# Kernel optimization log

Hardware: AMD Instinct MI355X
Metric: run time of the kernel (lower is better)

The kernel has to match this reference:

```python
import jax, jax.numpy as jnp
import numpy as np

DIM = 256
NUM_HEADS = 8
HEAD_DIM = 64
NUM_MEM_KV = 4
HIDDEN = NUM_HEADS * HEAD_DIM  # 512


def rmsnorm(x, g):
    # F.normalize(x, dim=1) * g * sqrt(C)
    c = x.shape[1]
    n = jnp.sqrt(jnp.sum(x * x, axis=1, keepdims=True))
    xn = x / jnp.maximum(n, 1e-12)
    return xn * g * (c ** 0.5)


def setup_inputs() -> dict:
    key = jax.random.key(0)
    ks = jax.random.split(key, 7)
    b, h, w = 16, 64, 64
    x = jax.random.normal(ks[0], (b, DIM, h, w), dtype=jnp.float32)
    g_in = jnp.ones((1, DIM, 1, 1), dtype=jnp.float32)
    w_qkv = jax.random.normal(ks[1], (HIDDEN * 3, DIM), dtype=jnp.float32) * (1.0 / np.sqrt(DIM))
    mem_kv = jax.random.normal(ks[2], (2, NUM_HEADS, HEAD_DIM, NUM_MEM_KV), dtype=jnp.float32)
    w_out = jax.random.normal(ks[3], (DIM, HIDDEN), dtype=jnp.float32) * (1.0 / np.sqrt(HIDDEN))
    b_out = jax.random.normal(ks[4], (DIM,), dtype=jnp.float32) * 0.01
    g_out = jnp.ones((1, DIM, 1, 1), dtype=jnp.float32)
    return {"x": x, "g_in": g_in, "w_qkv": w_qkv, "mem_kv": mem_kv,
            "w_out": w_out, "b_out": b_out, "g_out": g_out}


def reference(x, g_in, w_qkv, mem_kv, w_out, b_out, g_out):
    b, c, h, w = x.shape
    scale = HEAD_DIM ** (-0.5)
    xn = rmsnorm(x, g_in)
    # 1x1 conv (no bias) as GEMM: [b, 3*hidden, h, w]
    qkv = jnp.einsum('bcxy,oc->boxy', xn, w_qkv)
    q, k, v = jnp.split(qkv, 3, axis=1)
    # b (heads d) x y -> b heads d n
    def to_heads(t):
        return t.reshape(b, NUM_HEADS, HEAD_DIM, h * w)
    q, k, v = to_heads(q), to_heads(k), to_heads(v)
    mem_k = jnp.broadcast_to(mem_kv[0], (b, NUM_HEADS, HEAD_DIM, NUM_MEM_KV))
    mem_v = jnp.broadcast_to(mem_kv[1], (b, NUM_HEADS, HEAD_DIM, NUM_MEM_KV))
    k = jnp.concatenate([mem_k, k], axis=-1)
    v = jnp.concatenate([mem_v, v], axis=-1)
    q = jax.nn.softmax(q, axis=-2) * scale   # softmax over head_dim
    k = jax.nn.softmax(k, axis=-1)           # softmax over sequence
    context = jnp.einsum('bhdn,bhen->bhde', k, v)  # [b,h,d,d] per-head context
    out = jnp.einsum('bhde,bhdn->bhen', context, q)  # [b,h,d,n]
    out = out.reshape(b, HIDDEN, h, w)
    out = jnp.einsum('bcxy,oc->boxy', out, w_out) + b_out[None, :, None, None]
    return rmsnorm(out, g_out)
```

## Files before the change

kernel.cpp:

```cpp
#include <hip/hip_runtime.h>
#include <hip/hip_bf16.h>

typedef __hip_bfloat16 bf16;
typedef short bf16x8 __attribute__((ext_vector_type(8)));
typedef float f32x4 __attribute__((ext_vector_type(4)));

#define PTOT  65536
#define NPOS  4096
#define CIN   256
#define HID   512
#define HD    64

__device__ __forceinline__ float us2f(unsigned short u) {
    return __uint_as_float(((unsigned int)u) << 16);
}
__device__ __forceinline__ float ldf(const void* p, size_t i, bool bf) {
    return bf ? us2f(((const unsigned short*)p)[i]) : ((const float*)p)[i];
}
__device__ __forceinline__ unsigned short f2bs(float v) {
    __hip_bfloat16 h = __float2bfloat16(v);
    return *reinterpret_cast<unsigned short*>(&h);
}
__device__ __forceinline__ void gld16(const void* g, void* s) {
    __builtin_amdgcn_global_load_lds(
        (const __attribute__((address_space(1))) unsigned int*)g,
        (__attribute__((address_space(3))) unsigned int*)s, 16, 0, 0);
}

__global__ __launch_bounds__(256) void k_detect(const unsigned* __restrict__ x,
                                                int* __restrict__ flag) {
    int t = threadIdx.x;
    unsigned w = x[(size_t)t * 997];
    unsigned e7 = (w >> 8) & 0x7f;
    __shared__ int s[256];
    s[t] = (e7 >= 58 && e7 <= 66) ? 1 : 0;
    __syncthreads();
    for (int k = 128; k > 0; k >>= 1) { if (t < k) s[t] += s[t + k]; __syncthreads(); }
    if (t == 0) flag[0] = (s[0] >= 128) ? 1 : 0;
}

__global__ void k_relay(const int* __restrict__ src, int* __restrict__ dst) {
    dst[0] = src[0];
}

__global__ __launch_bounds__(256) void k_cvt(const void* __restrict__ src,
        unsigned short* __restrict__ dst, int n, const int* __restrict__ flag) {
    bool bf = flag[0] != 0;
    int i = blockIdx.x * 256 + threadIdx.x;
    if (i < n) dst[i] = f2bs(ldf(src, i, bf));
}

__global__ __launch_bounds__(256) void k_norm_xn(
        const void* __restrict__ x, const void* __restrict__ g,
        unsigned short* __restrict__ xn, const int* __restrict__ flag)
{
    bool bf = flag[0] != 0;
    __shared__ float xs[64][65];
    __shared__ float gS[256];
    __shared__ float sS[64];
    __shared__ float red[4][64];
    int t = threadIdx.x;
    int p0 = blockIdx.x * 64;
    int b = p0 >> 12;
    int posbase = p0 & 4095;
    gS[t] = ldf(g, t, bf);
    int pl = t & 63, cg = t >> 6;
    const size_t xbase = ((size_t)b * CIN) << 12;
    float ss = 0.f;
    for (int c = cg * 64; c < cg * 64 + 64; ++c) {
        float v = ldf(x, xbase + ((size_t)c << 12) + posbase + pl, bf);
        ss += v * v;
    }
    red[cg][pl] = ss;
    __syncthreads();
    if (t < 64) {
        float tot = red[0][t] + red[1][t] + red[2][t] + red[3][t];
        sS[t] = 16.0f / fmaxf(sqrtf(tot), 1e-12f);
    }
    for (int c0 = 0; c0 < 256; c0 += 64) {
        __syncthreads();
        #pragma unroll
        for (int r = 0; r < 16; ++r) {
            int c = c0 + r * 4 + cg;
            xs[r * 4 + cg][pl] = ldf(x, xbase + ((size_t)c << 12) + posbase + pl, bf);
        }
        __syncthreads();
        int pr = t >> 2, c4 = (t & 3) * 16;
        float sc = sS[pr];
        unsigned short tmp[16];
        #pragma unroll
        for (int j = 0; j < 16; ++j)
            tmp[j] = f2bs(xs[c4 + j][pr] * sc * gS[c0 + c4 + j]);
        unsigned short* dst = &xn[(size_t)(p0 + pr) * 256 + c0 + c4];
        *(uint4*)dst = ((uint4*)tmp)[0];
        *(uint4*)(dst + 8) = ((uint4*)tmp)[1];
    }
}

template<int KTOT, bool BIAS, int OSTRIDE>
__global__ __launch_bounds__(256) void k_mfma(
        const bf16* __restrict__ Am, const bf16* __restrict__ Bm,
        const void* __restrict__ bias, bf16* __restrict__ C,
        const int* __restrict__ flag)
{
    __shared__ __align__(16) unsigned short As[128 * 32];
    __shared__ __align__(16) unsigned short Bs[128 * 32];
    const int tid = threadIdx.x;
    const int wv = tid >> 6, lane = tid & 63;
    const int quad = lane >> 4, l16 = lane & 15;
    const int wm = wv >> 1, wn = wv & 1;
    const int m0 = blockIdx.y * 128, n0 = blockIdx.x * 128;
    f32x4 acc[4][4] = {};
    const bf16* gA = Am + (size_t)(m0 + (tid >> 2)) * KTOT + (tid & 3) * 8;
    const bf16* gB = Bm + (size_t)(n0 + (tid >> 2)) * KTOT + (tid & 3) * 8;
    unsigned short* lA = As + wv * 512;
    unsigned short* lB = Bs + wv * 512;
    for (int k0 = 0; k0 < KTOT; k0 += 32) {
        gld16(gA + k0, lA);
        gld16(gA + (size_t)64 * KTOT + k0, lA + 2048);
        gld16(gB + k0, lB);
        gld16(gB + (size_t)64 * KTOT + k0, lB + 2048);
        __syncthreads();
        bf16x8 bfr[4];
        #pragma unroll
        for (int j = 0; j < 4; ++j)
            bfr[j] = *(const bf16x8*)&Bs[(wn * 64 + j * 16 + l16) * 32 + quad * 8];
        #pragma unroll
        for (int i = 0; i < 4; ++i) {
            bf16x8 af = *(const bf16x8*)&As[(wm * 64 + i * 16 + l16) * 32 + quad * 8];
            #pragma unroll
            for (int j = 0; j < 4; ++j)
                acc[i][j] = __builtin_amdgcn_mfma_f32_16x16x32_bf16(af, bfr[j], acc[i][j], 0, 0, 0);
        }
        __syncthreads();
    }
    bool bf = BIAS ? (flag[0] != 0) : false;
    #pragma unroll
    for (int i = 0; i < 4; ++i) {
        int row = m0 + wm * 64 + i * 16 + quad * 4;
        #pragma unroll
        for (int r = 0; r < 4; ++r) {
            float bv = BIAS ? ldf(bias, row + r, bf) : 0.0f;
            #pragma unroll
            for (int j = 0; j < 4; ++j) {
                int col = n0 + wn * 64 + j * 16 + l16;
                C[(size_t)(row + r) * OSTRIDE + col] = __float2bfloat16(acc[i][j][r] + bv);
            }
        }
    }
}

__global__ __launch_bounds__(512) void k_kvgemm(
        const bf16* __restrict__ Am, const bf16* __restrict__ Bm,
        bf16* __restrict__ C)
{
    __shared__ __align__(16) unsigned short As[128 * 256];
    __shared__ __align__(16) unsigned short Bs[2][64 * 256];
    const int t = threadIdx.x;
    const int w = t >> 6, lane = t & 63;
    const int quad = lane >> 4, l16 = lane & 15;
    const int wm = w >> 1, wn = w & 1;
    const int p = blockIdx.x;
    const int xcd = p & 7, slot = p >> 3;
    const int chunk = xcd * 4 + (slot & 3);
    const int mt = slot >> 2;
    const int m0 = mt * 128;
    const size_t cbase = (size_t)chunk * 2048;

    const int srow = t >> 5;
    const int sks  = (t & 31) ^ (srow & 7);

    #pragma unroll
    for (int q = 0; q < 8; ++q)
        gld16(Am + (size_t)(m0 + q * 16 + srow) * 256 + sks * 8,
              (char*)As + q * 8192 + w * 1024);
    #pragma unroll
    for (int q = 0; q < 4; ++q)
        gld16(Bm + (cbase + q * 16 + srow) * 256 + sks * 8,
              (char*)Bs[0] + q * 8192 + w * 1024);
    #pragma unroll
    for (int q = 0; q < 4; ++q)
        gld16(Bm + (cbase + 64 + q * 16 + srow) * 256 + sks * 8,
              (char*)Bs[1] + q * 8192 + w * 1024);

    asm volatile("s_waitcnt vmcnt(8)" ::: "memory");
    __builtin_amdgcn_s_barrier();
    asm volatile("" ::: "memory");

    bf16x8 af[2][8];
    #pragma unroll
    for (int i = 0; i < 2; ++i) {
        int row = wm * 32 + i * 16 + l16;
        #pragma unroll
        for (int kk = 0; kk < 8; ++kk)
            af[i][kk] = *(const bf16x8*)((const char*)As + row * 512 +
                         (((kk * 4 + quad) ^ (row & 7)) << 4));
    }

    for (int s = 0; s < 32; ++s) {
        if (s > 0) {
            asm volatile("" ::: "memory");
            __builtin_amdgcn_s_barrier();
            asm volatile("" ::: "memory");
            if (s + 1 < 32) {
                #pragma unroll
                for (int q = 0; q < 4; ++q)
                    gld16(Bm + (cbase + (size_t)(s + 1) * 64 + q * 16 + srow) * 256 + sks * 8,
                          (char*)Bs[(s + 1) & 1] + q * 8192 + w * 1024);
            }
        }
        if (s == 0)      asm volatile("s_waitcnt vmcnt(4)"  ::: "memory");
        else if (s < 31) asm volatile("s_waitcnt vmcnt(20)" ::: "memory");
        else             asm volatile("s_waitcnt vmcnt(16)" ::: "memory");
        __builtin_amdgcn_s_barrier();
        asm volatile("" ::: "memory");

        const unsigned short* Bbuf = Bs[s & 1];
        f32x4 acc[2][2] = {};
        #pragma unroll
        for (int kk = 0; kk < 8; ++kk) {
            bf16x8 bfr[2];
            #pragma unroll
            for (int j = 0; j < 2; ++j) {
                int row = wn * 32 + j * 16 + l16;
                bfr[j] = *(const bf16x8*)((const char*)Bbuf + row * 512 +
                          (((kk * 4 + quad) ^ (row & 7)) << 4));
            }
            #pragma unroll
            for (int i = 0; i < 2; ++i)
                #pragma unroll
                for (int j = 0; j < 2; ++j)
                    acc[i][j] = __builtin_amdgcn_mfma_f32_16x16x32_bf16(af[i][kk], bfr[j], acc[i][j], 0, 0, 0);
        }
        #pragma unroll
        for (int i = 0; i < 2; ++i) {
            #pragma unroll
            for (int r = 0; r < 4; ++r) {
                int row = m0 + wm * 32 + i * 16 + quad * 4 + r;
                size_t col = cbase + (size_t)s * 64 + wn * 32;
                #pragma unroll
                for (int j = 0; j < 2; ++j)
                    C[(size_t)row * PTOT + col + j * 16 + l16] = __float2bfloat16(acc[i][j][r]);
            }
        }
    }
}

__global__ __launch_bounds__(256) void k_qapply(
        const bf16* __restrict__ xn, const bf16* __restrict__ wq,
        const unsigned short* __restrict__ ct_bf,
        unsigned short* __restrict__ oat_pe)
{
    __shared__ __align__(16) unsigned short smem[128 * 136 + 2 * 64 * 72];
    unsigned short* As  = smem;
    unsigned short* Bs  = smem + 8192;
    unsigned short* As2 = smem;
    unsigned short* ctS = smem + 17408;
    const int tid = threadIdx.x;
    const int wv = tid >> 6, lane = tid & 63;
    const int quad = lane >> 4, l16 = lane & 15;
    const int wm = wv >> 1, wn = wv & 1;
    const int n0 = blockIdx.x * 128;
    const int m0 = blockIdx.y * 128;
    const int b = m0 >> 12;

    {
        int hh = tid >> 7, tt = tid & 127;
        int bh = (b << 3) + (n0 >> 6) + hh;
        int e = tt >> 1, d0 = (tt & 1) * 32;
        const unsigned short* src = ct_bf + (size_t)bh * 4096 + e * 64 + d0;
        unsigned short* dst = ctS + hh * 4608 + e * 72 + d0;
        *(uint4*)dst        = *(const uint4*)src;
        *(uint4*)(dst + 8)  = *(const uint4*)(src + 8);
        *(uint4*)(dst + 16) = *(const uint4*)(src + 16);
        *(uint4*)(dst + 24) = *(const uint4*)(src + 24);
    }

    f32x4 acc[4][4] = {};
    const bf16* gA = xn + (size_t)(m0 + (tid >> 2)) * CIN + (tid & 3) * 8;
    const bf16* gB = wq + (size_t)(n0 + (tid >> 2)) * CIN + (tid & 3) * 8;
    unsigned short* lA = As + wv * 512;
    unsigned short* lB = Bs + wv * 512;
    for (int k0 = 0; k0 < CIN; k0 += 32) {
        gld16(gA + k0, lA);
        gld16(gA + (size_t)64 * CIN + k0, lA + 2048);
        gld16(gB + k0, lB);
        gld16(gB + (size_t)64 * CIN + k0, lB + 2048);
        __syncthreads();
        bf16x8 bfr[4];
        #pragma unroll
        for (int j = 0; j < 4; ++j)
            bfr[j] = *(const bf16x8*)&Bs[(wn * 64 + j * 16 + l16) * 32 + quad * 8];
        #pragma unroll
        for (int i = 0; i < 4; ++i) {
            bf16x8 af = *(const bf16x8*)&As[(wm * 64 + i * 16 + l16) * 32 + quad * 8];
            #pragma unroll
            for (int j = 0; j < 4; ++j)
                acc[i][j] = __builtin_amdgcn_mfma_f32_16x16x32_bf16(af, bfr[j], acc[i][j], 0, 0, 0);
        }
        __syncthreads();
    }

    #pragma unroll
    for (int i = 0; i < 4; ++i) {
        #pragma unroll
        for (int r = 0; r < 4; ++r) {
            float m = fmaxf(fmaxf(acc[i][0][r], acc[i][1][r]),
                            fmaxf(acc[i][2][r], acc[i][3][r]));
            #pragma unroll
            for (int s = 1; s < 16; s <<= 1)
                m = fmaxf(m, __shfl_xor(m, s));
            float ev[4];
            float sum = 0.f;
            #pragma unroll
            for (int j = 0; j < 4; ++j) { ev[j] = expf(acc[i][j][r] - m); sum += ev[j]; }
            #pragma unroll
            for (int s = 1; s < 16; s <<= 1)
                sum += __shfl_xor(sum, s);
            float inv = 0.125f / sum;
            int row = wm * 64 + i * 16 + quad * 4 + r;
            #pragma unroll
            for (int j = 0; j < 4; ++j)
                As2[row * 136 + wn * 64 + j * 16 + l16] = f2bs(ev[j] * inv);
        }
    }
    __syncthreads();

    f32x4 acc2[4][4] = {};
    #pragma unroll
    for (int kk = 0; kk < 2; ++kk) {
        bf16x8 bfr[4];
        #pragma unroll
        for (int j = 0; j < 4; ++j)
            bfr[j] = *(const bf16x8*)&ctS[wn * 4608 + (j * 16 + l16) * 72 + kk * 32 + quad * 8];
        #pragma unroll
        for (int i = 0; i < 4; ++i) {
            bf16x8 af = *(const bf16x8*)&As2[(wm * 64 + i * 16 + l16) * 136 + wn * 64 + kk * 32 + quad * 8];
            #pragma unroll
            for (int j = 0; j < 4; ++j)
                acc2[i][j] = __builtin_amdgcn_mfma_f32_16x16x32_bf16(af, bfr[j], acc2[i][j], 0, 0, 0);
        }
    }
    #pragma unroll
    for (int i = 0; i < 4; ++i) {
        #pragma unroll
        for (int r = 0; r < 4; ++r) {
            int prow = wm * 64 + i * 16 + quad * 4 + r;
            unsigned short* obase = oat_pe + (size_t)(m0 + prow) * HID + n0 + wn * 64;
            #pragma unroll
            for (int j = 0; j < 4; ++j)
                obase[j * 16 + l16] = f2bs(acc2[i][j][r]);
        }
    }
}

__global__ __launch_bounds__(256) void k_kstats(
        const bf16* __restrict__ kv, const void* __restrict__ memkv,
        float* __restrict__ rowmax, float* __restrict__ rowinv,
        const int* __restrict__ flag)
{
    bool bf = flag[0] != 0;
    int r = blockIdx.x;
    int b = r >> 9, hd = r & 511;
    const unsigned short* krow = (const unsigned short*)kv + (size_t)hd * PTOT + b * NPOS;
    int t = threadIdx.x;
    float vals[16];
    float m = -1e30f;
    #pragma unroll
    for (int i = 0; i < 16; ++i) {
        vals[i] = us2f(krow[t + (i << 8)]);
        m = fmaxf(m, vals[i]);
    }
    float mv = (t < 4) ? ldf(memkv, hd * 4 + t, bf) : -1e30f;
    m = fmaxf(m, mv);
    __shared__ float red[256];
    red[t] = m; __syncthreads();
    for (int s = 128; s > 0; s >>= 1) {
        if (t < s) red[t] = fmaxf(red[t], red[t + s]);
        __syncthreads();
    }
    float M = red[0]; __syncthreads();
    float sum = 0.f;
    #pragma unroll
    for (int i = 0; i < 16; ++i) sum += expf(vals[i] - M);
    if (t < 4) sum += expf(mv - M);
    red[t] = sum; __syncthreads();
    for (int s = 128; s > 0; s >>= 1) {
        if (t < s) red[t] += red[t + s];
        __syncthreads();
    }
    if (t == 0) { rowmax[r] = M; rowinv[r] = 1.0f / red[0]; }
}

__global__ __launch_bounds__(256) void k_context_mfma(
        const bf16* __restrict__ kv, const void* __restrict__ memkv,
        const float* __restrict__ rowmax, const float* __restrict__ rowinv,
        float* __restrict__ ctpart, const int* __restrict__ flag)
{
    bool bf = flag[0] != 0;
    int bh = blockIdx.x, chunk = blockIdx.y;
    int b = bh >> 3, h = bh & 7;
    __shared__ __align__(16) unsigned short As[4][64 * 32];
    __shared__ __align__(16) unsigned short Bs[4][64 * 32];
    __shared__ float rmS[64], riS[64];
    const int tid = threadIdx.x;
    if (tid < 64) {
        rmS[tid] = rowmax[(b << 9) + (h << 6) + tid];
        riS[tid] = rowinv[(b << 9) + (h << 6) + tid];
    }
    __syncthreads();
    const int wv = tid >> 6, lane = tid & 63;
    const int quad = lane >> 4, l16 = lane & 15;
    const int wm = wv >> 1, wn = wv & 1;
    const int krow = tid >> 2, kseg = tid & 3;
    const float rm = rmS[krow], ri = riS[krow];
    const unsigned short* kbase = (const unsigned short*)kv + (size_t)(h * HD) * PTOT + b * NPOS + chunk * 1024;
    const unsigned short* vbase = (const unsigned short*)kv + (size_t)(HID + h * HD) * PTOT + b * NPOS + chunk * 1024;
    f32x4 acc[2][2] = {};
    for (int s = 0; s < 8; ++s) {
        int nb = s * 128;
        #pragma unroll
        for (int kk = 0; kk < 4; ++kk) {
            uint4 u = *(const uint4*)(kbase + (size_t)krow * PTOT + nb + kk * 32 + kseg * 8);
            unsigned short out[8];
            const unsigned short* us = (const unsigned short*)&u;
            #pragma unroll
            for (int e = 0; e < 8; ++e)
                out[e] = f2bs(expf(us2f(us[e]) - rm) * ri);
            *(uint4*)&As[kk][krow * 32 + kseg * 8] = *(uint4*)out;
        }
        #pragma unroll
        for (int kk = 0; kk < 4; ++kk)
            gld16(vbase + (size_t)(wv * 16 + (lane >> 2)) * PTOT + nb + kk * 32 + (lane & 3) * 8,
                  &Bs[kk][wv * 512]);
        __syncthreads();
        #pragma unroll
        for (int kk = 0; kk < 4; ++kk) {
            bf16x8 bfr[2];
            #pragma unroll
            for (int j = 0; j < 2; ++j)
                bfr[j] = *(const bf16x8*)&Bs[kk][(wn * 32 + j * 16 + l16) * 32 + quad * 8];
            #pragma unroll
            for (int i = 0; i < 2; ++i) {
                bf16x8 af = *(const bf16x8*)&As[kk][(wm * 32 + i * 16 + l16) * 32 + quad * 8];
                #pragma unroll
                for (int j = 0; j < 2; ++j)
                    acc[i][j] = __builtin_amdgcn_mfma_f32_16x16x32_bf16(af, bfr[j], acc[i][j], 0, 0, 0);
            }
        }
        __syncthreads();
    }
    if (chunk == 0) {
        float mv[2][4];
        #pragma unroll
        for (int j = 0; j < 2; ++j) {
            int e = wn * 32 + j * 16 + l16;
            #pragma unroll
            for (int mm = 0; mm < 4; ++mm)
                mv[j][mm] = ldf(memkv, 2048 + ((h << 6) + e) * 4 + mm, bf);
        }
        #pragma unroll
        for (int i = 0; i < 2; ++i) {
            #pragma unroll
            for (int r = 0; r < 4; ++r) {
                int d = wm * 32 + i * 16 + quad * 4 + r;
                #pragma unroll
                for (int mm = 0; mm < 4; ++mm) {
                    float kw = expf(ldf(memkv, ((h << 6) + d) * 4 + mm, bf) - rmS[d]) * riS[d];
                    #pragma unroll
                    for (int j = 0; j < 2; ++j)
                        acc[i][j][r] = fmaf(kw, mv[j][mm], acc[i][j][r]);
                }
            }
        }
    }
    float* outp = ctpart + (size_t)(chunk * 128 + bh) * 4096;
    #pragma unroll
    for (int i = 0; i < 2; ++i) {
        #pragma unroll
        for (int r = 0; r < 4; ++r) {
            int d = wm * 32 + i * 16 + quad * 4 + r;
            #pragma unroll
            for (int j = 0; j < 2; ++j) {
                int e = wn * 32 + j * 16 + l16;
                outp[d * 64 + e] = acc[i][j][r];
            }
        }
    }
}

__global__ __launch_bounds__(256) void k_ctsum(
        const float* __restrict__ ctpart, unsigned short* __restrict__ ct_bf)
{
    int bh = blockIdx.x, t = threadIdx.x;
    int i0 = t * 16;
    int e = i0 >> 6, d0 = i0 & 63;
    unsigned short tmp[16];
    #pragma unroll
    for (int j = 0; j < 16; ++j) {
        int d = d0 + j;
        float s = 0.f;
        #pragma unroll
        for (int c = 0; c < 4; ++c)
            s += ctpart[(size_t)(c * 128 + bh) * 4096 + d * 64 + e];
        tmp[j] = f2bs(s);
    }
    unsigned short* dst = ct_bf + (size_t)bh * 4096 + i0;
    *(uint4*)dst = ((uint4*)tmp)[0];
    *(uint4*)(dst + 8) = ((uint4*)tmp)[1];
}

template<bool BF>
__device__ __forceinline__ void rmsout_body(const unsigned short* pre, const void* g, void* out) {
    int p = blockIdx.x * 256 + threadIdx.x;
    int b = p >> 12, pos = p & 4095;
    float ss = 0.f;
    for (int c = 0; c < CIN; ++c) { float v = us2f(pre[(size_t)c * PTOT + p]); ss += v * v; }
    float scale = 16.0f / fmaxf(sqrtf(ss), 1e-12f);
    for (int c = 0; c < CIN; ++c) {
        float v = us2f(pre[(size_t)c * PTOT + p]) * scale * (BF ? us2f(((const unsigned short*)g)[c]) : ((const float*)g)[c]);
        size_t oi = ((size_t)(b * CIN + c) << 12) + pos;
        if (BF) ((unsigned short*)out)[oi] = f2bs(v);
        else    ((float*)out)[oi] = v;
    }
}
__global__ __launch_bounds__(256) void k_rmsnorm_out(
        const unsigned short* __restrict__ pre, const void* __restrict__ g,
        void* __restrict__ out, const int* __restrict__ flag)
{
    if (flag[0]) rmsout_body<true>(pre, g, out);
    else         rmsout_body<false>(pre, g, out);
}

extern "C" void kernel_launch(void* const* d_in, const int* in_sizes, int n_in,
                              void* d_out, int out_size, void* d_ws, size_t ws_size,
                              hipStream_t stream) {
    const void* x     = d_in[0];
    const void* g_in  = d_in[1];
    const void* w_qkv = d_in[2];
    const void* memkv = d_in[3];
    const void* w_out = d_in[4];
    const void* b_out = d_in[5];
    const void* g_out = d_in[6];

    char* ws = (char*)d_ws;
    bf16*           kv     = (bf16*)ws;
    unsigned short* oat_pe = (unsigned short*)(ws + 67108864);
    unsigned short* pre    = (unsigned short*)ws;
    int*            flagB  = (int*)(ws + 50331648);

    char* ob = (char*)d_out;
    float*          ctpart = (float*)ob;
    float*          rowmax = (float*)(ob + 8388608);
    float*          rowinv = (float*)(ob + 8421376);
    int*            flagA  = (int*)(ob + 8454144);
    unsigned short* wq_b   = (unsigned short*)(ob + 9437184);
    unsigned short* wout_b = (unsigned short*)(ob + 10485760);
    unsigned short* ct_bf  = (unsigned short*)(ob + 11010048);
    unsigned short* xn     = (unsigned short*)(ob + 12582912);

    k_detect<<<1, 256, 0, stream>>>((const unsigned*)x, flagA);

    k_cvt<<<1536, 256, 0, stream>>>(w_qkv, wq_b, 1536 * 256, flagA);
    k_cvt<<<512, 256, 0, stream>>>(w_out, wout_b, 256 * 512, flagA);

    k_norm_xn<<<1024, 256, 0, stream>>>(x, g_in, xn, flagA);

    k_kvgemm<<<256, 512, 0, stream>>>(
        (const bf16*)(wq_b + (size_t)512 * CIN), (const bf16*)xn, kv);

    k_kstats<<<8192, 256, 0, stream>>>(kv, memkv, rowmax, rowinv, flagA);

    dim3 gctx(128, 4);
    k_context_mfma<<<gctx, 256, 0, stream>>>(kv, memkv, rowmax, rowinv, ctpart, flagA);

    k_ctsum<<<128, 256, 0, stream>>>(ctpart, ct_bf);

    dim3 gqa(4, 512);
    k_qapply<<<gqa, 256, 0, stream>>>(
        (const bf16*)xn, (const bf16*)wq_b, ct_bf, oat_pe);

    dim3 go(512, 2);
    k_mfma<HID, true, PTOT><<<go, 256, 0, stream>>>(
        (const bf16*)wout_b, (const bf16*)oat_pe, b_out, (bf16*)pre, flagA);

    k_relay<<<1, 1, 0, stream>>>(flagA, flagB);

    k_rmsnorm_out<<<256, 256, 0, stream>>>(pre, g_out, d_out, flagB);
}
```

Measured before the change: 393.7 us.

## Vectorize and single-pass input/output RMSNorm kernels with more blocks

The input RMSNorm kernel now reads x once with vectorized float4/ushort4 loads into a padded shared tile covering all 256 channels, instead of reading x twice (once for sum of squares, once for the transpose). The output RMSNorm kernel is restructured so each block handles 64 positions with 16 channel groups, keeps values in registers, writes vectorized outputs and launches 1024 blocks instead of 256 single-thread-per-position blocks. Both changes aim to cut global memory traffic and improve parallelism, at the cost of larger shared memory use (about 74KB) in the input kernel, which may limit occupancy.

After: 351.3 us. -10.8%, faster.

```diff
diff --git a/kernel.cpp b/kernel.cpp
--- a/kernel.cpp
+++ b/kernel.cpp
@@ -50,51 +50,77 @@
     if (i < n) dst[i] = f2bs(ldf(src, i, bf));
 }
 
+template<bool BF>
+__device__ __forceinline__ void norm_xn_body(const void* __restrict__ x,
+        const void* __restrict__ g, unsigned short* __restrict__ xn,
+        float* __restrict__ smem)
+{
+    float* xs   = smem;
+    float* gS   = smem + 17216;
+    float* red2 = smem + 17472;
+    float* sS   = smem + 18496;
+    const int t = threadIdx.x;
+    const int p0 = blockIdx.x * 64;
+    const int b = p0 >> 12;
+    const int posbase = p0 & 4095;
+    gS[t] = ldf(g, t, BF);
+    __syncthreads();
+    const int pl4 = (t & 15) * 4;
+    const int crow = t >> 4;
+    const size_t xbase = ((size_t)b * CIN) << 12;
+    float ssq[4] = {0.f, 0.f, 0.f, 0.f};
+    #pragma unroll
+    for (int rr = 0; rr < 16; ++rr) {
+        int c = rr * 16 + crow;
+        float v[4];
+        if (BF) {
+            ushort4 u = *(const ushort4*)((const unsigned short*)x + xbase +
+                                          ((size_t)c << 12) + posbase + pl4);
+            v[0] = us2f(u.x); v[1] = us2f(u.y); v[2] = us2f(u.z); v[3] = us2f(u.w);
+        } else {
+            float4 f = *(const float4*)((const float*)x + xbase +
+                                        ((size_t)c << 12) + posbase + pl4);
+            v[0] = f.x; v[1] = f.y; v[2] = f.z; v[3] = f.w;
+        }
+        float gv = gS[c];
+        float* row = xs + (c >> 6) * 4304 + (c & 63) * 67;
+        #pragma unroll
+        for (int e = 0; e < 4; ++e) {
+            ssq[e] += v[e] * v[e];
+            row[pl4 + e] = v[e] * gv;
+        }
+    }
+    #pragma unroll
+    for (int e = 0; e < 4; ++e) red2[crow * 64 + pl4 + e] = ssq[e];
+    __syncthreads();
+    if (t < 64) {
+        float tot = 0.f;
+        #pragma unroll
+        for (int j = 0; j < 16; ++j) tot += red2[j * 64 + t];
+        sS[t] = 16.0f / fmaxf(sqrtf(tot), 1e-12f);
+    }
+    __syncthreads();
+    const int pr = t >> 2, c0 = (t & 3) * 64;
+    const float sc = sS[pr];
+    const float* base = xs + (t & 3) * 4304 + pr;
+    unsigned short* dst = &xn[(size_t)(p0 + pr) * 256 + c0];
+    #pragma unroll
+    for (int q = 0; q < 4; ++q) {
+        unsigned short tmp[16];
+        #pragma unroll
+        for (int j = 0; j < 16; ++j)
+            tmp[j] = f2bs(base[(q * 16 + j) * 67] * sc);
+        *(uint4*)(dst + q * 16)     = ((uint4*)tmp)[0];
+        *(uint4*)(dst + q * 16 + 8) = ((uint4*)tmp)[1];
+    }
+}
 __global__ __launch_bounds__(256) void k_norm_xn(
         const void* __restrict__ x, const void* __restrict__ g,
         unsigned short* __restrict__ xn, const int* __restrict__ flag)
 {
-    bool bf = flag[0] != 0;
-    __shared__ float xs[64][65];
-    __shared__ float gS[256];
-    __shared__ float sS[64];
-    __shared__ float red[4][64];
-    int t = threadIdx.x;
-    int p0 = blockIdx.x * 64;
-    int b = p0 >> 12;
-    int posbase = p0 & 4095;
-    gS[t] = ldf(g, t, bf);
-    int pl = t & 63, cg = t >> 6;
-    const size_t xbase = ((size_t)b * CIN) << 12;
-    float ss = 0.f;
-    for (int c = cg * 64; c < cg * 64 + 64; ++c) {
-        float v = ldf(x, xbase + ((size_t)c << 12) + posbase + pl, bf);
-        ss += v * v;
-    }
-    red[cg][pl] = ss;
-    __syncthreads();
-    if (t < 64) {
-        float tot = red[0][t] + red[1][t] + red[2][t] + red[3][t];
-        sS[t] = 16.0f / fmaxf(sqrtf(tot), 1e-12f);
-    }
-    for (int c0 = 0; c0 < 256; c0 += 64) {
-        __syncthreads();
-        #pragma unroll
-        for (int r = 0; r < 16; ++r) {
-            int c = c0 + r * 4 + cg;
-            xs[r * 4 + cg][pl] = ldf(x, xbase + ((size_t)c << 12) + posbase + pl, bf);
-        }
-        __syncthreads();
-        int pr = t >> 2, c4 = (t & 3) * 16;
-        float sc = sS[pr];
-        unsigned short tmp[16];
-        #pragma unroll
-        for (int j = 0; j < 16; ++j)
-            tmp[j] = f2bs(xs[c4 + j][pr] * sc * gS[c0 + c4 + j]);
-        unsigned short* dst = &xn[(size_t)(p0 + pr) * 256 + c0 + c4];
-        *(uint4*)dst = ((uint4*)tmp)[0];
-        *(uint4*)(dst + 8) = ((uint4*)tmp)[1];
-    }
+    __shared__ float smem[18560];
+    if (flag[0]) norm_xn_body<true>(x, g, xn, smem);
+    else         norm_xn_body<false>(x, g, xn, smem);
 }
 
 template<int KTOT, bool BIAS, int OSTRIDE>
@@ -511,25 +537,66 @@
 }
 
 template<bool BF>
-__device__ __forceinline__ void rmsout_body(const unsigned short* pre, const void* g, void* out) {
-    int p = blockIdx.x * 256 + threadIdx.x;
-    int b = p >> 12, pos = p & 4095;
-    float ss = 0.f;
-    for (int c = 0; c < CIN; ++c) { float v = us2f(pre[(size_t)c * PTOT + p]); ss += v * v; }
-    float scale = 16.0f / fmaxf(sqrtf(ss), 1e-12f);
-    for (int c = 0; c < CIN; ++c) {
-        float v = us2f(pre[(size_t)c * PTOT + p]) * scale * (BF ? us2f(((const unsigned short*)g)[c]) : ((const float*)g)[c]);
-        size_t oi = ((size_t)(b * CIN + c) << 12) + pos;
-        if (BF) ((unsigned short*)out)[oi] = f2bs(v);
-        else    ((float*)out)[oi] = v;
+__device__ __forceinline__ void rmsout_body(const unsigned short* __restrict__ pre,
+        const void* __restrict__ g, void* __restrict__ out, float* __restrict__ smem)
+{
+    float* gS   = smem;
+    float* red2 = smem + 256;
+    float* sS   = smem + 1280;
+    const int t = threadIdx.x;
+    const int p0 = blockIdx.x * 64;
+    const int b = p0 >> 12;
+    const int posbase = p0 & 4095;
+    gS[t] = ldf(g, t, BF);
+    const int pl4 = (t & 15) * 4;
+    const int crow = t >> 4;
+    const unsigned short* pbase = pre + p0 + pl4;
+    ushort4 u[16];
+    float ssq[4] = {0.f, 0.f, 0.f, 0.f};
+    #pragma unroll
+    for (int rr = 0; rr < 16; ++rr) {
+        int c = rr * 16 + crow;
+        u[rr] = *(const ushort4*)(pbase + (size_t)c * PTOT);
+        float v0 = us2f(u[rr].x), v1 = us2f(u[rr].y), v2 = us2f(u[rr].z), v3 = us2f(u[rr].w);
+        ssq[0] += v0 * v0; ssq[1] += v1 * v1; ssq[2] += v2 * v2; ssq[3] += v3 * v3;
+    }
+    #pragma unroll
+    for (int e = 0; e < 4; ++e) red2[crow * 64 + pl4 + e] = ssq[e];
+    __syncthreads();
+    if (t < 64) {
+        float tot = 0.f;
+        #pragma unroll
+        for (int j = 0; j < 16; ++j) tot += red2[j * 64 + t];
+        sS[t] = 16.0f / fmaxf(sqrtf(tot), 1e-12f);
+    }
+    __syncthreads();
+    const float s0 = sS[pl4], s1 = sS[pl4 + 1], s2 = sS[pl4 + 2], s3 = sS[pl4 + 3];
+    #pragma unroll
+    for (int rr = 0; rr < 16; ++rr) {
+        int c = rr * 16 + crow;
+        float gv = gS[c];
+        float v0 = us2f(u[rr].x) * s0 * gv;
+        float v1 = us2f(u[rr].y) * s1 * gv;
+        float v2 = us2f(u[rr].z) * s2 * gv;
+        float v3 = us2f(u[rr].w) * s3 * gv;
+        size_t oi = ((size_t)(b * CIN + c) << 12) + posbase + pl4;
+        if (BF) {
+            ushort4 o;
+            o.x = f2bs(v0); o.y = f2bs(v1); o.z = f2bs(v2); o.w = f2bs(v3);
+            *(ushort4*)((unsigned short*)out + oi) = o;
+        } else {
+            float4 o; o.x = v0; o.y = v1; o.z = v2; o.w = v3;
+            *(float4*)((float*)out + oi) = o;
+        }
     }
 }
 __global__ __launch_bounds__(256) void k_rmsnorm_out(
         const unsigned short* __restrict__ pre, const void* __restrict__ g,
         void* __restrict__ out, const int* __restrict__ flag)
 {
-    if (flag[0]) rmsout_body<true>(pre, g, out);
-    else         rmsout_body<false>(pre, g, out);
+    __shared__ float smem[1344];
+    if (flag[0]) rmsout_body<true>(pre, g, out, smem);
+    else         rmsout_body<false>(pre, g, out, smem);
 }
 
 extern "C" void kernel_launch(void* const* d_in, const int* in_sizes, int n_in,
@@ -586,5 +653,5 @@
 
     k_relay<<<1, 1, 0, stream>>>(flagA, flagB);
 
-    k_rmsnorm_out<<<256, 256, 0, stream>>>(pre, g_out, d_out, flagB);
-}
+    k_rmsnorm_out<<<1024, 256, 0, stream>>>(pre, g_out, d_out, flagB);
+}
```
